# Performance work log

Hardware: AMD Instinct MI355X
Metric: run time of the kernel (lower is better)

## Reference

```python
import jax, jax.numpy as jnp
import numpy as np

MARGIN = 0.3
NORM = 2.0  # p-norm used by both pairwise() and PairwiseDistance

M, C = 65536, 256   # n*h*w pixels, feature channels
K, P, Q = 20, 2048, 2048  # classes 1..nclass-1, positives, negatives per class


def setup_inputs() -> dict:
    key = jax.random.key(0)
    k1, k2, k3 = jax.random.split(key, 3)
    features = jax.random.normal(k1, (M, C), dtype=jnp.float32)
    pos_idx = jax.random.randint(k2, (K, P), 0, M)
    neg_idx = jax.random.randint(k3, (K, Q), 0, M)
    return {"features": features, "pos_idx": pos_idx, "neg_idx": neg_idx}


def _pairwise(x, y):
    # torch: clamp(xx - 2xy + yy, 0); (dis + eps) ** (1/norm)
    eps = 0.0001 / x.shape[1]
    xx = jnp.sum(x * x, axis=1)           # [P]
    yy = jnp.sum(y * y, axis=1)           # [Q]
    xy = x @ y.T                           # [P,Q] GEMM
    dis = jnp.clip(xx[:, None] - 2.0 * xy + yy[None, :], 0.0)
    return (dis + eps) ** (1.0 / NORM)


def _pdist(x1, x2):
    # PairwiseDistance: (clamp(sum(|x1-x2|^p), 0) + eps) ** (1/p)
    eps = 0.0001 / x1.shape[1]
    out = jnp.sum(jnp.abs(x1 - x2) ** NORM, axis=1)
    return (jnp.clip(out, 0.0) + eps) ** (1.0 / NORM)


def _class_loss(pos, neg):
    # hard mining on detached features (indices only, as in generate_triplet_simple)
    pos_d = jax.lax.stop_gradient(pos)
    neg_d = jax.lax.stop_gradient(neg)
    hp = jnp.argmax(_pairwise(pos_d, pos_d), axis=1)   # hardest positive per anchor
    hn = jnp.argmin(_pairwise(pos_d, neg_d), axis=1)   # hardest negative per anchor
    d_p = _pdist(pos, pos[hp])
    d_n = _pdist(pos, neg[hn])
    return jnp.mean(jnp.clip(MARGIN + d_p - d_n, 0.0))


def reference(features, pos_idx, neg_idx):
    f = jax.nn.sigmoid(features)          # torch.sigmoid(features)
    pos = f[pos_idx]                      # [K,P,C]
    neg = f[neg_idx]                      # [K,Q,C]
    losses = jax.vmap(_class_loss)(pos, neg)  # per-class triplet losses
    return jnp.sum(losses)                # loss accumulated over classes
```

## Files before the change

kernel.cpp:

```cpp
#include <hip/hip_runtime.h>
#include <stdint.h>

#define M_ROWS 65536
#define C_DIM  256
#define K_CLS  20
#define P_POS  2048
#define MARGIN_F 0.3f
#define EPS_D (0.0001f / 256.0f)
#define SCALE1 0x7F7F7F7Fu

typedef float floatx4 __attribute__((ext_vector_type(4)));
typedef int   intx8   __attribute__((ext_vector_type(8)));
union Frag8 { intx8 v; uint4 q[2]; };

__device__ __forceinline__ void async_copy16(const void* g, void* l) {
    __builtin_amdgcn_global_load_lds(
        (const __attribute__((address_space(1))) void*)g,
        (__attribute__((address_space(3))) void*)l, 16, 0, 0);
}
__device__ __forceinline__ float sigm(float x) { return 1.f / (1.f + __expf(-x)); }

__global__ __launch_bounds__(256) void sigmoid_norm_k(
        const float* __restrict__ feat,
        unsigned int* __restrict__ S8,
        float* __restrict__ xx,
        unsigned int* __restrict__ hp,
        unsigned int* __restrict__ hn) {
    {
        const int idx = blockIdx.x * 256 + threadIdx.x;
        if (idx < K_CLS * P_POS) { hp[idx] = 0u; hn[idx] = 0xFFFFFFFFu; }
    }
    const int wave = threadIdx.x >> 6, lane = threadIdx.x & 63;
    const int row = blockIdx.x * 4 + wave;
    const float4 v = *(const float4*)(feat + (size_t)row * C_DIM + lane * 4);

    const int p01 = __builtin_amdgcn_cvt_pk_fp8_f32(sigm(v.x), sigm(v.y), 0, false);
    const int p23 = __builtin_amdgcn_cvt_pk_fp8_f32(sigm(v.z), sigm(v.w), 0, false);
    const unsigned int packed = (unsigned int)(p01 & 0xFFFF) | ((unsigned int)p23 << 16);
    S8[(size_t)row * 64 + lane] = packed;

    const float q0 = __builtin_amdgcn_cvt_f32_fp8(p01, 0);
    const float q1 = __builtin_amdgcn_cvt_f32_fp8(p01, 1);
    const float q2 = __builtin_amdgcn_cvt_f32_fp8(p23, 0);
    const float q3 = __builtin_amdgcn_cvt_f32_fp8(p23, 1);
    float sum = q0 * q0 + q1 * q1 + q2 * q2 + q3 * q3;
#pragma unroll
    for (int off = 32; off; off >>= 1) sum += __shfl_down(sum, off);
    if (lane == 0) xx[row] = sum;
}

__global__ __launch_bounds__(256, 3) void select_k(
        const unsigned int* __restrict__ S8,
        const float* __restrict__ xx,
        const int* __restrict__ pos_idx,
        const int* __restrict__ neg_idx,
        unsigned int* __restrict__ hp,
        unsigned int* __restrict__ hn) {
    __shared__ __align__(16) unsigned char Bt[2][32 * 256];

    const int tid    = threadIdx.x;
    const int w      = tid >> 6;
    const int lane   = tid & 63;
    const int lane15 = lane & 15;
    const int quad   = lane >> 4;

    const int bid    = blockIdx.x;
    const int ctid   = bid % 40;
    const int rest   = bid / 40;
    const int i_blk  = rest >> 2;
    const int jq     = rest & 3;
    const int k      = ctid >> 1;
    const int isNeg  = ctid & 1;
    const int i0     = i_blk * 256;
    const int j0     = jq * 512;

    const int* __restrict__ idxA = pos_idx + k * P_POS;
    const int* __restrict__ idxB = (isNeg ? neg_idx : pos_idx) + k * P_POS;
    unsigned int* outKey         = (isNeg ? hn : hp) + k * P_POS;

    const char* S8B = (const char*)S8;

    const int rl  = lane >> 4;
    const int cch = lane & 15;
    int rloc[2], soff[2];
#pragma unroll
    for (int c = 0; c < 2; ++c) {
        rloc[c] = (w * 2 + c) * 4 + rl;
        soff[c] = (cch ^ (rloc[c] & 15)) << 4;
    }

    int g_st[2];
#pragma unroll
    for (int c = 0; c < 2; ++c) g_st[c] = idxB[j0 + rloc[c]];
#pragma unroll
    for (int c = 0; c < 2; ++c)
        async_copy16(S8B + ((size_t)(uint32_t)g_st[c] << 8) + soff[c],
                     (char*)&Bt[0][0] + (w * 2 + c) * 1024);
#pragma unroll
    for (int c = 0; c < 2; ++c) g_st[c] = idxB[j0 + 32 + rloc[c]];

    float yv0 = xx[idxB[j0 + lane15]];
    float yv1 = xx[idxB[j0 + 16 + lane15]];
    int idx_n0 = idxB[j0 + 32 + lane15];
    int idx_n1 = idxB[j0 + 48 + lane15];

    Frag8 A_reg[4][2];
#pragma unroll
    for (int si = 0; si < 4; ++si) {
        const int gi = idxA[i0 + w * 64 + si * 16 + lane15];
        const char* rb = S8B + ((size_t)(uint32_t)gi << 8) + quad * 32;
#pragma unroll
        for (int s = 0; s < 2; ++s) {
            A_reg[si][s].q[0] = *(const uint4*)(rb + s * 128);
            A_reg[si][s].q[1] = *(const uint4*)(rb + s * 128 + 16);
        }
    }

    int blo[2], bhi[2];
#pragma unroll
    for (int s = 0; s < 2; ++s) {
        const int c0 = s * 8 + quad * 2;
        blo[s] = lane15 * 256 + ((c0 ^ lane15) << 4);
        bhi[s] = lane15 * 256 + (((c0 + 1) ^ lane15) << 4);
    }

    float bestv[16];
    const float binit = isNeg ? 3.4e38f : -3.4e38f;
#pragma unroll
    for (int t = 0; t < 16; ++t) bestv[t] = binit;

#pragma unroll 2
    for (int jc = 0; jc < 16; ++jc) {
        __syncthreads();

        const float nv0 = xx[idx_n0];
        const float nv1 = xx[idx_n1];

        if (jc < 15) {
            char* lb = (char*)(&Bt[(jc + 1) & 1][0]);
#pragma unroll
            for (int c = 0; c < 2; ++c)
                async_copy16(S8B + ((size_t)(uint32_t)g_st[c] << 8) + soff[c],
                             lb + (w * 2 + c) * 1024);
        }
        {
            const int nt = j0 + (jc < 14 ? jc + 2 : 15) * 32;
#pragma unroll
            for (int c = 0; c < 2; ++c) g_st[c] = idxB[nt + rloc[c]];
            idx_n0 = idxB[nt + lane15];
            idx_n1 = idxB[nt + 16 + lane15];
        }

        const char* Bb = (const char*)(&Bt[jc & 1][0]);
        floatx4 acc[2][4];
#pragma unroll
        for (int ct = 0; ct < 2; ++ct)
#pragma unroll
            for (int si = 0; si < 4; ++si)
                acc[ct][si] = (floatx4){0.f, 0.f, 0.f, 0.f};

#pragma unroll
        for (int s = 0; s < 2; ++s) {
            Frag8 bf0, bf1;
            bf0.q[0] = *(const uint4*)(Bb + blo[s]);
            bf0.q[1] = *(const uint4*)(Bb + bhi[s]);
            bf1.q[0] = *(const uint4*)(Bb + blo[s] + 4096);
            bf1.q[1] = *(const uint4*)(Bb + bhi[s] + 4096);
#pragma unroll
            for (int si = 0; si < 4; ++si)
                acc[0][si] = __builtin_amdgcn_mfma_scale_f32_16x16x128_f8f6f4(
                    A_reg[si][s].v, bf0.v, acc[0][si], 0, 0,
                    0, SCALE1, 0, SCALE1);
#pragma unroll
            for (int si = 0; si < 4; ++si)
                acc[1][si] = __builtin_amdgcn_mfma_scale_f32_16x16x128_f8f6f4(
                    A_reg[si][s].v, bf1.v, acc[1][si], 0, 0,
                    0, SCALE1, 0, SCALE1);
        }

        const uint32_t jb0 = (uint32_t)((j0 + (jc << 5)) | lane15);
        const uint32_t jb1 = jb0 | 16u;
#pragma unroll
        for (int ct = 0; ct < 2; ++ct) {
            const float yv = ct ? yv1 : yv0;
            const uint32_t jb = ct ? jb1 : jb0;
#pragma unroll
            for (int si = 0; si < 4; ++si)
#pragma unroll
                for (int r = 0; r < 4; ++r) {
                    const float g = fmaf(-2.f, acc[ct][si][r], yv);
                    const float enc = __uint_as_float(
                        (__float_as_uint(g) & 0xFFFFF800u) | jb);
                    const int slot = si * 4 + r;
                    bestv[slot] = isNeg ? fminf(bestv[slot], enc)
                                        : fmaxf(bestv[slot], enc);
                }
        }
        yv0 = nv0; yv1 = nv1;
    }

#pragma unroll
    for (int slot = 0; slot < 16; ++slot) {
#pragma unroll
        for (int off = 1; off < 16; off <<= 1) {
            const float ov = __shfl_xor(bestv[slot], off);
            bestv[slot] = isNeg ? fminf(bestv[slot], ov) : fmaxf(bestv[slot], ov);
        }
    }
    if (lane15 == 0) {
#pragma unroll
        for (int si = 0; si < 4; ++si)
#pragma unroll
            for (int r = 0; r < 4; ++r) {
                const int row = w * 64 + si * 16 + quad * 4 + r;
                const uint32_t u = __float_as_uint(bestv[si * 4 + r]);
                const uint32_t key = (u & 0x80000000u) ? ~u : (u | 0x80000000u);
                if (isNeg) atomicMin(&outKey[i0 + row], key);
                else       atomicMax(&outKey[i0 + row], key);
            }
    }
}

__global__ __launch_bounds__(256) void loss_k(
        const unsigned int* __restrict__ S8,
        const int* __restrict__ pos_idx,
        const int* __restrict__ neg_idx,
        const unsigned int* __restrict__ hp,
        const unsigned int* __restrict__ hn,
        float* __restrict__ terms) {
    const int wave = threadIdx.x >> 6, lane = threadIdx.x & 63;
    const int a = blockIdx.x * 4 + wave;
    const int k = a >> 11;
    const int i = a & 2047;
    const int* pidx = pos_idx + (k << 11);
    const int* nidx = neg_idx + (k << 11);
    const unsigned int kp = hp[a], kn = hn[a];
    const int jp = (int)((kp & 0x80000000u) ? (kp & 2047u) : ((~kp) & 2047u));
    const int jn = (int)((kn & 0x80000000u) ? (kn & 2047u) : ((~kn) & 2047u));
    const int ga = pidx[i];
    const int gp = pidx[jp];
    const int gn = nidx[jn];

    const int wa = (int)S8[(size_t)ga * 64 + lane];
    const int wp = (int)S8[(size_t)gp * 64 + lane];
    const int wn = (int)S8[(size_t)gn * 64 + lane];

    float dp = 0.f, dn = 0.f;
    {
        float xa, d;
        xa = __builtin_amdgcn_cvt_f32_fp8(wa, 0);
        d = xa - __builtin_amdgcn_cvt_f32_fp8(wp, 0); dp += d * d;
        d = xa - __builtin_amdgcn_cvt_f32_fp8(wn, 0); dn += d * d;
        xa = __builtin_amdgcn_cvt_f32_fp8(wa, 1);
        d = xa - __builtin_amdgcn_cvt_f32_fp8(wp, 1); dp += d * d;
        d = xa - __builtin_amdgcn_cvt_f32_fp8(wn, 1); dn += d * d;
        xa = __builtin_amdgcn_cvt_f32_fp8(wa, 2);
        d = xa - __builtin_amdgcn_cvt_f32_fp8(wp, 2); dp += d * d;
        d = xa - __builtin_amdgcn_cvt_f32_fp8(wn, 2); dn += d * d;
        xa = __builtin_amdgcn_cvt_f32_fp8(wa, 3);
        d = xa - __builtin_amdgcn_cvt_f32_fp8(wp, 3); dp += d * d;
        d = xa - __builtin_amdgcn_cvt_f32_fp8(wn, 3); dn += d * d;
    }
#pragma unroll
    for (int off = 32; off; off >>= 1) {
        dp += __shfl_down(dp, off);
        dn += __shfl_down(dn, off);
    }
    if (lane == 0) {
        const float d_p = sqrtf(fmaxf(dp, 0.f) + EPS_D);
        const float d_n = sqrtf(fmaxf(dn, 0.f) + EPS_D);
        terms[a] = fmaxf(MARGIN_F + d_p - d_n, 0.f);
    }
}

__global__ __launch_bounds__(1024) void reduce_k(
        const float* __restrict__ terms, float* __restrict__ out) {
    __shared__ float red[1024];
    float s = 0.f;
    for (int i = threadIdx.x; i < K_CLS * P_POS; i += 1024) s += terms[i];
    red[threadIdx.x] = s;
    __syncthreads();
    for (int off = 512; off; off >>= 1) {
        if ((int)threadIdx.x < off) red[threadIdx.x] += red[threadIdx.x + off];
        __syncthreads();
    }
    if (threadIdx.x == 0) out[0] = red[0] * (1.0f / (float)P_POS);
}

extern "C" void kernel_launch(void* const* d_in, const int* in_sizes, int n_in,
                              void* d_out, int out_size, void* d_ws, size_t ws_size,
                              hipStream_t stream) {
    const float* feat    = (const float*)d_in[0];
    const int*   pos_idx = (const int*)d_in[1];
    const int*   neg_idx = (const int*)d_in[2];

    char* ws = (char*)d_ws;
    unsigned int* S8 = (unsigned int*)ws;
    float*        xx = (float*)(ws + 16777216);
    unsigned int* hp = (unsigned int*)(ws + 17039360);
    unsigned int* hn = (unsigned int*)(ws + 17203200);
    float*     terms = (float*)(ws + 17367040);

    sigmoid_norm_k<<<M_ROWS / 4, 256, 0, stream>>>(feat, S8, xx, hp, hn);

    select_k<<<32 * 40, 256, 0, stream>>>(S8, xx, pos_idx, neg_idx, hp, hn);

    loss_k<<<(K_CLS * P_POS) / 4, 256, 0, stream>>>(S8, pos_idx, neg_idx, hp, hn, terms);

    reduce_k<<<1, 1024, 0, stream>>>(terms, (float*)d_out);
}
```

Measured before the change: 186.4 us.

## Switch hard-mining GEMM from 16x16x128 to 32x32x64 scaled FP8 MFMA

Reworks the select_k inner product to use the 32x32x64 scaled f8f6f4 MFMA instead of the 16x16x128 variant. Each wave now holds two 32-row A tiles over four K-steps, and reads one B fragment per step that both MFMAs share. This cuts LDS fragment reads and the instruction count per tile. The cost is a 32-entry running min/max per lane, a wider shuffle reduction, and the removal of the unroll-2 pragma, which raises register pressure under the 3-blocks-per-CU launch bound.

```diff
diff --git a/kernel.cpp b/kernel.cpp
--- a/kernel.cpp
+++ b/kernel.cpp
@@ -9,8 +9,8 @@
 #define EPS_D (0.0001f / 256.0f)
 #define SCALE1 0x7F7F7F7Fu
 
-typedef float floatx4 __attribute__((ext_vector_type(4)));
-typedef int   intx8   __attribute__((ext_vector_type(8)));
+typedef float floatx16 __attribute__((ext_vector_type(16)));
+typedef int   intx8    __attribute__((ext_vector_type(8)));
 union Frag8 { intx8 v; uint4 q[2]; };
 
 __device__ __forceinline__ void async_copy16(const void* g, void* l) {
@@ -61,8 +61,8 @@
     const int tid    = threadIdx.x;
     const int w      = tid >> 6;
     const int lane   = tid & 63;
-    const int lane15 = lane & 15;
-    const int quad   = lane >> 4;
+    const int lane31 = lane & 31;
+    const int half   = lane >> 5;
 
     const int bid    = blockIdx.x;
     const int ctid   = bid % 40;
@@ -99,42 +99,38 @@
 #pragma unroll
     for (int c = 0; c < 2; ++c) g_st[c] = idxB[j0 + 32 + rloc[c]];
 
-    float yv0 = xx[idxB[j0 + lane15]];
-    float yv1 = xx[idxB[j0 + 16 + lane15]];
-    int idx_n0 = idxB[j0 + 32 + lane15];
-    int idx_n1 = idxB[j0 + 48 + lane15];
-
-    Frag8 A_reg[4][2];
-#pragma unroll
-    for (int si = 0; si < 4; ++si) {
-        const int gi = idxA[i0 + w * 64 + si * 16 + lane15];
-        const char* rb = S8B + ((size_t)(uint32_t)gi << 8) + quad * 32;
-#pragma unroll
-        for (int s = 0; s < 2; ++s) {
-            A_reg[si][s].q[0] = *(const uint4*)(rb + s * 128);
-            A_reg[si][s].q[1] = *(const uint4*)(rb + s * 128 + 16);
-        }
-    }
-
-    int blo[2], bhi[2];
-#pragma unroll
-    for (int s = 0; s < 2; ++s) {
-        const int c0 = s * 8 + quad * 2;
-        blo[s] = lane15 * 256 + ((c0 ^ lane15) << 4);
-        bhi[s] = lane15 * 256 + (((c0 + 1) ^ lane15) << 4);
-    }
-
-    float bestv[16];
+    float yv  = xx[idxB[j0 + lane31]];
+    int idx_n = idxB[j0 + 32 + lane31];
+
+    Frag8 A_reg[2][4];
+#pragma unroll
+    for (int t = 0; t < 2; ++t) {
+        const int gi = idxA[i0 + w * 64 + t * 32 + lane31];
+        const char* rb = S8B + ((size_t)(uint32_t)gi << 8) + half * 32;
+#pragma unroll
+        for (int s = 0; s < 4; ++s) {
+            A_reg[t][s].q[0] = *(const uint4*)(rb + s * 64);
+            A_reg[t][s].q[1] = *(const uint4*)(rb + s * 64 + 16);
+        }
+    }
+
+    int blo[4], bhi[4];
+#pragma unroll
+    for (int s = 0; s < 4; ++s) {
+        const int c0 = s * 4 + half * 2;
+        blo[s] = lane31 * 256 + ((c0 ^ (lane31 & 15)) << 4);
+        bhi[s] = lane31 * 256 + (((c0 + 1) ^ (lane31 & 15)) << 4);
+    }
+
+    float bestv[32];
     const float binit = isNeg ? 3.4e38f : -3.4e38f;
 #pragma unroll
-    for (int t = 0; t < 16; ++t) bestv[t] = binit;
-
-#pragma unroll 2
+    for (int t = 0; t < 32; ++t) bestv[t] = binit;
+
     for (int jc = 0; jc < 16; ++jc) {
         __syncthreads();
 
-        const float nv0 = xx[idx_n0];
-        const float nv1 = xx[idx_n1];
+        const float nv = xx[idx_n];
 
         if (jc < 15) {
             char* lb = (char*)(&Bt[(jc + 1) & 1][0]);
@@ -147,73 +143,57 @@
             const int nt = j0 + (jc < 14 ? jc + 2 : 15) * 32;
 #pragma unroll
             for (int c = 0; c < 2; ++c) g_st[c] = idxB[nt + rloc[c]];
-            idx_n0 = idxB[nt + lane15];
-            idx_n1 = idxB[nt + 16 + lane15];
+            idx_n = idxB[nt + lane31];
         }
 
         const char* Bb = (const char*)(&Bt[jc & 1][0]);
-        floatx4 acc[2][4];
-#pragma unroll
-        for (int ct = 0; ct < 2; ++ct)
-#pragma unroll
-            for (int si = 0; si < 4; ++si)
-                acc[ct][si] = (floatx4){0.f, 0.f, 0.f, 0.f};
-
-#pragma unroll
-        for (int s = 0; s < 2; ++s) {
-            Frag8 bf0, bf1;
-            bf0.q[0] = *(const uint4*)(Bb + blo[s]);
-            bf0.q[1] = *(const uint4*)(Bb + bhi[s]);
-            bf1.q[0] = *(const uint4*)(Bb + blo[s] + 4096);
-            bf1.q[1] = *(const uint4*)(Bb + bhi[s] + 4096);
-#pragma unroll
-            for (int si = 0; si < 4; ++si)
-                acc[0][si] = __builtin_amdgcn_mfma_scale_f32_16x16x128_f8f6f4(
-                    A_reg[si][s].v, bf0.v, acc[0][si], 0, 0,
-                    0, SCALE1, 0, SCALE1);
-#pragma unroll
-            for (int si = 0; si < 4; ++si)
-                acc[1][si] = __builtin_amdgcn_mfma_scale_f32_16x16x128_f8f6f4(
-                    A_reg[si][s].v, bf1.v, acc[1][si], 0, 0,
-                    0, SCALE1, 0, SCALE1);
-        }
-
-        const uint32_t jb0 = (uint32_t)((j0 + (jc << 5)) | lane15);
-        const uint32_t jb1 = jb0 | 16u;
-#pragma unroll
-        for (int ct = 0; ct < 2; ++ct) {
-            const float yv = ct ? yv1 : yv0;
-            const uint32_t jb = ct ? jb1 : jb0;
-#pragma unroll
-            for (int si = 0; si < 4; ++si)
-#pragma unroll
-                for (int r = 0; r < 4; ++r) {
-                    const float g = fmaf(-2.f, acc[ct][si][r], yv);
-                    const float enc = __uint_as_float(
-                        (__float_as_uint(g) & 0xFFFFF800u) | jb);
-                    const int slot = si * 4 + r;
-                    bestv[slot] = isNeg ? fminf(bestv[slot], enc)
-                                        : fmaxf(bestv[slot], enc);
-                }
-        }
-        yv0 = nv0; yv1 = nv1;
-    }
-
-#pragma unroll
-    for (int slot = 0; slot < 16; ++slot) {
-#pragma unroll
-        for (int off = 1; off < 16; off <<= 1) {
+        floatx16 acc0 = {0.f}, acc1 = {0.f};
+#pragma unroll
+        for (int s = 0; s < 4; ++s) {
+            Frag8 bf;
+            bf.q[0] = *(const uint4*)(Bb + blo[s]);
+            bf.q[1] = *(const uint4*)(Bb + bhi[s]);
+            acc0 = __builtin_amdgcn_mfma_scale_f32_32x32x64_f8f6f4(
+                A_reg[0][s].v, bf.v, acc0, 0, 0, 0, SCALE1, 0, SCALE1);
+            acc1 = __builtin_amdgcn_mfma_scale_f32_32x32x64_f8f6f4(
+                A_reg[1][s].v, bf.v, acc1, 0, 0, 0, SCALE1, 0, SCALE1);
+        }
+
+        const uint32_t jb = (uint32_t)(j0 + (jc << 5) + lane31);
+#pragma unroll
+        for (int r = 0; r < 16; ++r) {
+            {
+                const float g = fmaf(-2.f, acc0[r], yv);
+                const float enc = __uint_as_float(
+                    (__float_as_uint(g) & 0xFFFFF800u) | jb);
+                bestv[r] = isNeg ? fminf(bestv[r], enc) : fmaxf(bestv[r], enc);
+            }
+            {
+                const float g = fmaf(-2.f, acc1[r], yv);
+                const float enc = __uint_as_float(
+                    (__float_as_uint(g) & 0xFFFFF800u) | jb);
+                bestv[16 + r] = isNeg ? fminf(bestv[16 + r], enc)
+                                      : fmaxf(bestv[16 + r], enc);
+            }
+        }
+        yv = nv;
+    }
+
+#pragma unroll
+    for (int slot = 0; slot < 32; ++slot) {
+#pragma unroll
+        for (int off = 1; off < 32; off <<= 1) {
             const float ov = __shfl_xor(bestv[slot], off);
             bestv[slot] = isNeg ? fminf(bestv[slot], ov) : fmaxf(bestv[slot], ov);
         }
     }
-    if (lane15 == 0) {
-#pragma unroll
-        for (int si = 0; si < 4; ++si)
-#pragma unroll
-            for (int r = 0; r < 4; ++r) {
-                const int row = w * 64 + si * 16 + quad * 4 + r;
-                const uint32_t u = __float_as_uint(bestv[si * 4 + r]);
+    if (lane31 == 0) {
+#pragma unroll
+        for (int t = 0; t < 2; ++t)
+#pragma unroll
+            for (int r = 0; r < 16; ++r) {
+                const int row = w * 64 + t * 32 + (r & 3) + 8 * (r >> 2) + 4 * half;
+                const uint32_t u = __float_as_uint(bestv[t * 16 + r]);
                 const uint32_t key = (u & 0x80000000u) ? ~u : (u | 0x80000000u);
                 if (isNeg) atomicMin(&outKey[i0 + row], key);
                 else       atomicMax(&outKey[i0 + row], key);
```

Result: slower. 214.7 us (+15.2%).
